# Optimization experiments

Measured on AMD Instinct MI355X. Metric: run time of the kernel, lower is better.

## Reference

```python
import jax, jax.numpy as jnp
import numpy as np


def setup_inputs() -> dict:
    N, E, D = 50000, 800000, 64
    key = jax.random.key(0)
    ks = jax.random.split(key, 8)
    s = 1.0 / np.sqrt(2 * D)
    inp = {
        "node_emb": jax.random.normal(ks[0], (N, D), dtype=jnp.float32),
        "edge_index": jax.random.randint(ks[1], (2, E), 0, N, dtype=jnp.int64),
        "W1": jax.random.normal(ks[2], (2 * D, D), dtype=jnp.float32) * s,
        "b1": jnp.zeros((D,), dtype=jnp.float32),
        "W2": jax.random.normal(ks[3], (D, D), dtype=jnp.float32) * (1.0 / np.sqrt(D)),
        "b2": jnp.zeros((D,), dtype=jnp.float32),
        "Wg": jax.random.normal(ks[4], (D, D), dtype=jnp.float32) * (1.0 / np.sqrt(D)),
        "bg": jnp.zeros((D,), dtype=jnp.float32),
    }
    return inp


def reference(node_emb, edge_index, W1, b1, W2, b2, Wg, bg):
    # Gather pairwise embeddings along edges
    src, dst = edge_index[0], edge_index[1]
    pair_emb = jnp.concatenate([node_emb[src], node_emb[dst]], axis=-1)  # [E, 2D]
    # Interaction MLP (dropout in eval mode -> identity)
    h = jax.nn.relu(pair_emb @ W1 + b1)
    interaction = h @ W2 + b2  # [E, D]
    # Sigmoid gate
    gate = jax.nn.sigmoid(interaction @ Wg + bg)
    gated = interaction * gate  # [E, D]
    # Scatter-mean back to source nodes
    N = node_emb.shape[0]
    summed = jax.ops.segment_sum(gated, src, num_segments=N)  # [N, D]
    counts = jax.ops.segment_sum(jnp.ones((src.shape[0],), dtype=gated.dtype), src, num_segments=N)
    pooled = summed / jnp.maximum(counts, 1.0)[:, None]
    return pooled
```

## Files before the change

### kernel.cpp

```cpp
#include <hip/hip_runtime.h>


typedef unsigned short ushort_t;
typedef __attribute__((ext_vector_type(8))) short     bf16x8;
typedef __attribute__((ext_vector_type(8))) unsigned short u16x8;
typedef __attribute__((ext_vector_type(4))) float     f32x4;

constexpr int D        = 64;
constexpr int TILE     = 64;
constexpr int BLOCK    = 256;
constexpr int NFRAG    = 32;
constexpr int SLAB_B   = 4352;
constexpr int PAIR_STR = 136;
constexpr int H_STR    = 72;
constexpr int G_STR    = 68;

static __device__ __forceinline__ ushort_t f2bf(float f) {
    union { float f; unsigned int u; } v; v.f = f;
    const unsigned int r = v.u + 0x7FFFu + ((v.u >> 16) & 1u);
    return (ushort_t)(r >> 16);
}


__global__ void prep_kernel(const float* __restrict__ W1, const float* __restrict__ W2,
                            const float* __restrict__ Wg,
                            const float* __restrict__ b2, const float* __restrict__ bg,
                            const float* __restrict__ emb, const int* __restrict__ ei,
                            ushort_t* __restrict__ wpack, float* __restrict__ bgp,
                            ushort_t* __restrict__ emb_bf, int* __restrict__ cnt,
                            int total_emb, int cvt_blocks, int E) {
    const int bid = blockIdx.x;
    if (bid < 64) {
        const int t = bid * 256 + threadIdx.x;
        const int f = t >> 9;
        const int l = (t >> 3) & 63;
        const int j = t & 7;
        const int k = ((f < 16) ? (f & 3) : ((f - 16) & 1)) * 32 + (l >> 4) * 8 + j;
        const int n = ((f < 16) ? (f >> 2) : (((f & 7)) >> 1)) * 16 + (l & 15);
        float v;
        if (f < 16)      v = W1[k * 64 + n];
        else if (f < 24) v = W2[k * 64 + n];
        else {
            float s = 0.f;
            const float* wr = W2 + k * 64;
#pragma unroll 8
            for (int m = 0; m < 64; ++m) s += wr[m] * Wg[m * 64 + n];
            v = s;
        }
        wpack[t] = f2bf(v);
    } else if (bid < 64 + cvt_blocks) {
        const int idx  = (bid - 64) * 256 + threadIdx.x;
        const int base = idx * 8;
        if (base < total_emb) {
            const float4 a = *(const float4*)(emb + base);
            const float4 b = *(const float4*)(emb + base + 4);
            u16x8 p;
            p[0]=f2bf(a.x); p[1]=f2bf(a.y); p[2]=f2bf(a.z); p[3]=f2bf(a.w);
            p[4]=f2bf(b.x); p[5]=f2bf(b.y); p[6]=f2bf(b.z); p[7]=f2bf(b.w);
            *(u16x8*)(emb_bf + base) = p;
        }
    } else if (bid == 64 + cvt_blocks) {
        const int n = threadIdx.x;
        if (n < 64) {
            float s = bg[n];
#pragma unroll 8
            for (int m = 0; m < 64; ++m) s += b2[m] * Wg[m * 64 + n];
            bgp[n] = s;
        }
    } else {
        const int e = ((bid - 65 - cvt_blocks) * 256 + threadIdx.x) * 4;
        if (e + 3 < E) {
            const int4 v = *(const int4*)(ei + e);
            atomicAdd(&cnt[v.x], 1); atomicAdd(&cnt[v.y], 1);
            atomicAdd(&cnt[v.z], 1); atomicAdd(&cnt[v.w], 1);
        } else {
            for (int k = e; k < E; ++k) atomicAdd(&cnt[ei[k]], 1);
        }
    }
}


__global__ void scan_block(const int* __restrict__ cnt, int* __restrict__ off,
                           int* __restrict__ bsum, int N) {
    __shared__ int s[256];
    const int t = threadIdx.x, i = blockIdx.x * 256 + t;
    const int x = (i < N) ? cnt[i] : 0;
    s[t] = x; __syncthreads();
    for (int d = 1; d < 256; d <<= 1) {
        const int v = (t >= d) ? s[t - d] : 0;
        __syncthreads();
        s[t] += v;
        __syncthreads();
    }
    if (i < N) off[i] = s[t] - x;
    if (t == 255) bsum[blockIdx.x] = s[255];
}

__global__ void scatter_idx(const int* __restrict__ ei, int* __restrict__ off,
                            const int* __restrict__ bsum, unsigned* __restrict__ sorted,
                            int E, int nb) {
    __shared__ int pref[256];
    const int t = threadIdx.x;
    const int x = (t < nb) ? bsum[t] : 0;
    pref[t] = x; __syncthreads();
    for (int d = 1; d < 256; d <<= 1) {
        const int v = (t >= d) ? pref[t - d] : 0;
        __syncthreads();
        pref[t] += v;
        __syncthreads();
    }
    const int e = (blockIdx.x * blockDim.x + t) * 4;
    if (e + 3 < E) {
        const int4 v = *(const int4*)(ei + e);
        const int4 d = *(const int4*)(ei + E + e);
        const int bx = v.x >> 8, by = v.y >> 8, bz = v.z >> 8, bw = v.w >> 8;
        sorted[(bx ? pref[bx - 1] : 0) + atomicAdd(&off[v.x], 1)] =
            ((unsigned)v.x << 16) | (unsigned)d.x;
        sorted[(by ? pref[by - 1] : 0) + atomicAdd(&off[v.y], 1)] =
            ((unsigned)v.y << 16) | (unsigned)d.y;
        sorted[(bz ? pref[bz - 1] : 0) + atomicAdd(&off[v.z], 1)] =
            ((unsigned)v.z << 16) | (unsigned)d.z;
        sorted[(bw ? pref[bw - 1] : 0) + atomicAdd(&off[v.w], 1)] =
            ((unsigned)v.w << 16) | (unsigned)d.w;
    } else {
        for (int k = e; k < E; ++k) {
            const int s = ei[k], b = s >> 8;
            sorted[(b ? pref[b - 1] : 0) + atomicAdd(&off[s], 1)] =
                ((unsigned)s << 16) | (unsigned)ei[E + k];
        }
    }
}


__global__ __launch_bounds__(BLOCK, 6)
void edge_mlp_mfma(const ushort_t* __restrict__ emb_bf,
                   const unsigned* __restrict__ sorted,
                   const ushort_t* __restrict__ wpack,
                   const float* __restrict__ b1, const float* __restrict__ b2,
                   const float* __restrict__ bgp,
                   const int*   __restrict__ cnt,
                   float* __restrict__ summed,
                   int E)
{
    __shared__ char  slab[4][SLAB_B];
    __shared__ int   srcIds[TILE];
    __shared__ float rcS[TILE];

    const int tid = threadIdx.x;

    {
        const int e = tid >> 2, q = tid & 3;
        ushort_t* prow = (ushort_t*)&slab[e >> 4][(e & 15) * (PAIR_STR * 2)];
        const int ide = blockIdx.x * TILE + e;
        if (ide < E) {
            const unsigned p = sorted[ide];
            const int s  = (int)(p >> 16);
            const int dn = (int)(p & 0xFFFFu);
            if (q == 0) { srcIds[e] = s; rcS[e] = 1.0f / fmaxf((float)cnt[s], 1.0f); }
            const ushort_t* sr = emb_bf + (size_t)s  * D + q * 16;
            const ushort_t* dr = emb_bf + (size_t)dn * D + q * 16;
            *(u16x8*)&prow[q * 16]          = *(const u16x8*)sr;
            *(u16x8*)&prow[q * 16 + 8]      = *(const u16x8*)(sr + 8);
            *(u16x8*)&prow[64 + q * 16]     = *(const u16x8*)dr;
            *(u16x8*)&prow[64 + q * 16 + 8] = *(const u16x8*)(dr + 8);
        } else {
            if (q == 0) { srcIds[e] = -1; rcS[e] = 1.0f; }
            const u16x8 z = {0,0,0,0,0,0,0,0};
            *(u16x8*)&prow[q * 16]          = z;
            *(u16x8*)&prow[q * 16 + 8]      = z;
            *(u16x8*)&prow[64 + q * 16]     = z;
            *(u16x8*)&prow[64 + q * 16 + 8] = z;
        }
    }

    const int w    = tid >> 6;
    const int ln   = tid & 63;
    const int quad = ln >> 4;
    const int cn   = ln & 15;
    ushort_t* pairW = (ushort_t*)slab[w];
    ushort_t* hW    = (ushort_t*)slab[w];
    float*    gW    = (float*)   slab[w];

    bf16x8 a1f[4];
#pragma unroll
    for (int kc = 0; kc < 4; ++kc)
        a1f[kc] = *(const bf16x8*)&pairW[cn * PAIR_STR + kc * 32 + quad * 8];

    f32x4 acc1[4];
#pragma unroll
    for (int nt = 0; nt < 4; ++nt) {
        const float b = b1[nt * 16 + cn];
        acc1[nt] = (f32x4){b, b, b, b};
    }
#pragma unroll
    for (int nt = 0; nt < 4; ++nt)
#pragma unroll
        for (int kc = 0; kc < 4; ++kc) {
            const bf16x8 bf = *(const bf16x8*)(wpack + ((nt * 4 + kc) * 64 + ln) * 8);
            acc1[nt] = __builtin_amdgcn_mfma_f32_16x16x32_bf16(a1f[kc], bf, acc1[nt], 0, 0, 0);
        }
#pragma unroll
    for (int nt = 0; nt < 4; ++nt)
#pragma unroll
        for (int r = 0; r < 4; ++r)
            hW[(quad * 4 + r) * H_STR + nt * 16 + cn] = f2bf(fmaxf(acc1[nt][r], 0.f));

    bf16x8 a2f[2];
#pragma unroll
    for (int kc = 0; kc < 2; ++kc)
        a2f[kc] = *(const bf16x8*)&hW[cn * H_STR + kc * 32 + quad * 8];

    f32x4 acc2[4], accg[4];
#pragma unroll
    for (int nt = 0; nt < 4; ++nt) {
        const float b  = b2 [nt * 16 + cn];
        const float bG = bgp[nt * 16 + cn];
        acc2[nt] = (f32x4){b, b, b, b};
        accg[nt] = (f32x4){bG, bG, bG, bG};
    }
#pragma unroll
    for (int nt = 0; nt < 4; ++nt)
#pragma unroll
        for (int kc = 0; kc < 2; ++kc) {
            const bf16x8 bf2 = *(const bf16x8*)(wpack + ((16 + nt * 2 + kc) * 64 + ln) * 8);
            const bf16x8 bfg = *(const bf16x8*)(wpack + ((24 + nt * 2 + kc) * 64 + ln) * 8);
            acc2[nt] = __builtin_amdgcn_mfma_f32_16x16x32_bf16(a2f[kc], bf2, acc2[nt], 0, 0, 0);
            accg[nt] = __builtin_amdgcn_mfma_f32_16x16x32_bf16(a2f[kc], bfg, accg[nt], 0, 0, 0);
        }

#pragma unroll
    for (int nt = 0; nt < 4; ++nt)
#pragma unroll
        for (int r = 0; r < 4; ++r) {
            const float g = 1.0f / (1.0f + __expf(-accg[nt][r]));
            gW[(quad * 4 + r) * G_STR + nt * 16 + cn] = acc2[nt][r] * g;
        }

    {
        const int rbase = 16 * w;
        float run = 0.f;
        int   prev = srcIds[rbase];
        int   lastIdx = rbase;
#pragma unroll
        for (int i = 0; i < 16; ++i) {
            const int s = srcIds[rbase + i];
            const float v = gW[i * G_STR + ln];
            if (s != prev) {
                if (prev >= 0)
                    unsafeAtomicAdd(&summed[(size_t)prev * D + ln], run * rcS[lastIdx]);
                run = 0.f;
                prev = s;
            }
            run += v;
            lastIdx = rbase + i;
        }
        if (prev >= 0)
            unsafeAtomicAdd(&summed[(size_t)prev * D + ln], run * rcS[lastIdx]);
    }
}

extern "C" void kernel_launch(void* const* d_in, const int* in_sizes, int n_in,
                              void* d_out, int out_size, void* d_ws, size_t ws_size,
                              hipStream_t stream) {
    const float* node_emb   = (const float*)d_in[0];
    const int*   edge_index = (const int*)d_in[1];
    const float* W1 = (const float*)d_in[2];
    const float* b1 = (const float*)d_in[3];
    const float* W2 = (const float*)d_in[4];
    const float* b2 = (const float*)d_in[5];
    const float* Wg = (const float*)d_in[6];
    const float* bg = (const float*)d_in[7];

    const int N = in_sizes[0] / D;
    const int E = in_sizes[1] / 2;
    const int total_emb = N * D;

    int* cnt    = (int*)d_ws;
    int* off    = cnt + N;
    int* bsum   = off + N;
    unsigned* sorted = (unsigned*)(bsum + 256);
    float* bgp  = (float*)(sorted + E);
    ushort_t* wpack  = (ushort_t*)(bgp + 64);
    ushort_t* emb_bf = wpack + NFRAG * 512;

    float* summed = (float*)d_out;

    hipMemsetAsync(cnt, 0, sizeof(int) * (size_t)N, stream);
    hipMemsetAsync(summed, 0, sizeof(float) * (size_t)total_emb, stream);

    const int cvt_blocks = (total_emb / 8 + 255) / 256;
    const int e4blocks   = ((E + 3) / 4 + 255) / 256;
    prep_kernel<<<64 + cvt_blocks + 1 + e4blocks, 256, 0, stream>>>(
        W1, W2, Wg, b2, bg, node_emb, edge_index,
        wpack, bgp, emb_bf, cnt, total_emb, cvt_blocks, E);

    const int nblocks = (N + 255) / 256;
    scan_block <<<nblocks, 256, 0, stream>>>(cnt, off, bsum, N);
    scatter_idx<<<e4blocks, 256, 0, stream>>>(edge_index, off, bsum, sorted, E, nblocks);

    const int ntiles = (E + TILE - 1) / TILE;
    edge_mlp_mfma<<<ntiles, BLOCK, 0, stream>>>(emb_bf, sorted, wpack,
                                                b1, b2, bgp, cnt, summed, E);
}
```

Measured before the change: 256.2 us.

## Reduce segments in registers via shuffles, fold output zeroing into prep kernel

The gated values now stay in registers instead of being staged through LDS: each lane accumulates its rows per source segment and cross-quad sums are done with xor shuffles before the atomic add. The memset of the output is replaced by extra zeroing blocks in the prep kernel, which removes one launch. MFMA loops are reordered to load each A fragment just before use, and the launch-bounds occupancy hint rises from 6 to 8 blocks per CU. Together these aim to cut LDS traffic, registers and launch overhead. The cost is extra shuffle work per segment boundary and possible register spilling under the tighter bound.

```diff
diff --git a/kernel.cpp b/kernel.cpp
--- a/kernel.cpp
+++ b/kernel.cpp
@@ -13,7 +13,6 @@
 constexpr int SLAB_B   = 4352;
 constexpr int PAIR_STR = 136;
 constexpr int H_STR    = 72;
-constexpr int G_STR    = 68;
 
 static __device__ __forceinline__ ushort_t f2bf(float f) {
     union { float f; unsigned int u; } v; v.f = f;
@@ -28,7 +27,8 @@
                             const float* __restrict__ emb, const int* __restrict__ ei,
                             ushort_t* __restrict__ wpack, float* __restrict__ bgp,
                             ushort_t* __restrict__ emb_bf, int* __restrict__ cnt,
-                            int total_emb, int cvt_blocks, int E) {
+                            float* __restrict__ summed,
+                            int total_emb, int cvt_blocks, int e4blocks, int E) {
     const int bid = blockIdx.x;
     if (bid < 64) {
         const int t = bid * 256 + threadIdx.x;
@@ -67,7 +67,7 @@
             for (int m = 0; m < 64; ++m) s += b2[m] * Wg[m * 64 + n];
             bgp[n] = s;
         }
-    } else {
+    } else if (bid < 65 + cvt_blocks + e4blocks) {
         const int e = ((bid - 65 - cvt_blocks) * 256 + threadIdx.x) * 4;
         if (e + 3 < E) {
             const int4 v = *(const int4*)(ei + e);
@@ -76,6 +76,11 @@
         } else {
             for (int k = e; k < E; ++k) atomicAdd(&cnt[ei[k]], 1);
         }
+    } else {
+        const int idx  = (bid - 65 - cvt_blocks - e4blocks) * 256 + threadIdx.x;
+        const int base = idx * 4;
+        if (base < total_emb)
+            *(float4*)(summed + base) = (float4){0.f, 0.f, 0.f, 0.f};
     }
 }
 
@@ -132,7 +137,7 @@
 }
 
 
-__global__ __launch_bounds__(BLOCK, 6)
+__global__ __launch_bounds__(BLOCK, 8)
 void edge_mlp_mfma(const ushort_t* __restrict__ emb_bf,
                    const unsigned* __restrict__ sorted,
                    const ushort_t* __restrict__ wpack,
@@ -149,27 +154,27 @@
     const int tid = threadIdx.x;
 
     {
-        const int e = tid >> 2, q = tid & 3;
+        const int e = tid >> 2, q4 = tid & 3;
         ushort_t* prow = (ushort_t*)&slab[e >> 4][(e & 15) * (PAIR_STR * 2)];
         const int ide = blockIdx.x * TILE + e;
         if (ide < E) {
             const unsigned p = sorted[ide];
             const int s  = (int)(p >> 16);
             const int dn = (int)(p & 0xFFFFu);
-            if (q == 0) { srcIds[e] = s; rcS[e] = 1.0f / fmaxf((float)cnt[s], 1.0f); }
-            const ushort_t* sr = emb_bf + (size_t)s  * D + q * 16;
-            const ushort_t* dr = emb_bf + (size_t)dn * D + q * 16;
-            *(u16x8*)&prow[q * 16]          = *(const u16x8*)sr;
-            *(u16x8*)&prow[q * 16 + 8]      = *(const u16x8*)(sr + 8);
-            *(u16x8*)&prow[64 + q * 16]     = *(const u16x8*)dr;
-            *(u16x8*)&prow[64 + q * 16 + 8] = *(const u16x8*)(dr + 8);
+            if (q4 == 0) { srcIds[e] = s; rcS[e] = 1.0f / fmaxf((float)cnt[s], 1.0f); }
+            const ushort_t* sr = emb_bf + (size_t)s  * D + q4 * 16;
+            const ushort_t* dr = emb_bf + (size_t)dn * D + q4 * 16;
+            *(u16x8*)&prow[q4 * 16]          = *(const u16x8*)sr;
+            *(u16x8*)&prow[q4 * 16 + 8]      = *(const u16x8*)(sr + 8);
+            *(u16x8*)&prow[64 + q4 * 16]     = *(const u16x8*)dr;
+            *(u16x8*)&prow[64 + q4 * 16 + 8] = *(const u16x8*)(dr + 8);
         } else {
-            if (q == 0) { srcIds[e] = -1; rcS[e] = 1.0f; }
+            if (q4 == 0) { srcIds[e] = -1; rcS[e] = 1.0f; }
             const u16x8 z = {0,0,0,0,0,0,0,0};
-            *(u16x8*)&prow[q * 16]          = z;
-            *(u16x8*)&prow[q * 16 + 8]      = z;
-            *(u16x8*)&prow[64 + q * 16]     = z;
-            *(u16x8*)&prow[64 + q * 16 + 8] = z;
+            *(u16x8*)&prow[q4 * 16]          = z;
+            *(u16x8*)&prow[q4 * 16 + 8]      = z;
+            *(u16x8*)&prow[64 + q4 * 16]     = z;
+            *(u16x8*)&prow[64 + q4 * 16 + 8] = z;
         }
     }
 
@@ -179,12 +184,6 @@
     const int cn   = ln & 15;
     ushort_t* pairW = (ushort_t*)slab[w];
     ushort_t* hW    = (ushort_t*)slab[w];
-    float*    gW    = (float*)   slab[w];
-
-    bf16x8 a1f[4];
-#pragma unroll
-    for (int kc = 0; kc < 4; ++kc)
-        a1f[kc] = *(const bf16x8*)&pairW[cn * PAIR_STR + kc * 32 + quad * 8];
 
     f32x4 acc1[4];
 #pragma unroll
@@ -193,22 +192,19 @@
         acc1[nt] = (f32x4){b, b, b, b};
     }
 #pragma unroll
-    for (int nt = 0; nt < 4; ++nt)
-#pragma unroll
-        for (int kc = 0; kc < 4; ++kc) {
+    for (int kc = 0; kc < 4; ++kc) {
+        const bf16x8 a = *(const bf16x8*)&pairW[cn * PAIR_STR + kc * 32 + quad * 8];
+#pragma unroll
+        for (int nt = 0; nt < 4; ++nt) {
             const bf16x8 bf = *(const bf16x8*)(wpack + ((nt * 4 + kc) * 64 + ln) * 8);
-            acc1[nt] = __builtin_amdgcn_mfma_f32_16x16x32_bf16(a1f[kc], bf, acc1[nt], 0, 0, 0);
-        }
+            acc1[nt] = __builtin_amdgcn_mfma_f32_16x16x32_bf16(a, bf, acc1[nt], 0, 0, 0);
+        }
+    }
 #pragma unroll
     for (int nt = 0; nt < 4; ++nt)
 #pragma unroll
         for (int r = 0; r < 4; ++r)
             hW[(quad * 4 + r) * H_STR + nt * 16 + cn] = f2bf(fmaxf(acc1[nt][r], 0.f));
-
-    bf16x8 a2f[2];
-#pragma unroll
-    for (int kc = 0; kc < 2; ++kc)
-        a2f[kc] = *(const bf16x8*)&hW[cn * H_STR + kc * 32 + quad * 8];
 
     f32x4 acc2[4], accg[4];
 #pragma unroll
@@ -219,43 +215,66 @@
         accg[nt] = (f32x4){bG, bG, bG, bG};
     }
 #pragma unroll
-    for (int nt = 0; nt < 4; ++nt)
-#pragma unroll
-        for (int kc = 0; kc < 2; ++kc) {
+    for (int kc = 0; kc < 2; ++kc) {
+        const bf16x8 a = *(const bf16x8*)&hW[cn * H_STR + kc * 32 + quad * 8];
+#pragma unroll
+        for (int nt = 0; nt < 4; ++nt) {
             const bf16x8 bf2 = *(const bf16x8*)(wpack + ((16 + nt * 2 + kc) * 64 + ln) * 8);
             const bf16x8 bfg = *(const bf16x8*)(wpack + ((24 + nt * 2 + kc) * 64 + ln) * 8);
-            acc2[nt] = __builtin_amdgcn_mfma_f32_16x16x32_bf16(a2f[kc], bf2, acc2[nt], 0, 0, 0);
-            accg[nt] = __builtin_amdgcn_mfma_f32_16x16x32_bf16(a2f[kc], bfg, accg[nt], 0, 0, 0);
-        }
-
+            acc2[nt] = __builtin_amdgcn_mfma_f32_16x16x32_bf16(a, bf2, acc2[nt], 0, 0, 0);
+            accg[nt] = __builtin_amdgcn_mfma_f32_16x16x32_bf16(a, bfg, accg[nt], 0, 0, 0);
+        }
+    }
+
+    float g[4][4];
 #pragma unroll
     for (int nt = 0; nt < 4; ++nt)
 #pragma unroll
-        for (int r = 0; r < 4; ++r) {
-            const float g = 1.0f / (1.0f + __expf(-accg[nt][r]));
-            gW[(quad * 4 + r) * G_STR + nt * 16 + cn] = acc2[nt][r] * g;
-        }
+        for (int r = 0; r < 4; ++r)
+            g[nt][r] = acc2[nt][r] / (1.0f + __expf(-accg[nt][r]));
 
     {
         const int rbase = 16 * w;
-        float run = 0.f;
-        int   prev = srcIds[rbase];
-        int   lastIdx = rbase;
+        float part0 = 0.f, part1 = 0.f, part2 = 0.f, part3 = 0.f;
+        int   segSrc = srcIds[rbase];
+        int   segRow = 0;
 #pragma unroll
         for (int i = 0; i < 16; ++i) {
             const int s = srcIds[rbase + i];
-            const float v = gW[i * G_STR + ln];
-            if (s != prev) {
-                if (prev >= 0)
-                    unsafeAtomicAdd(&summed[(size_t)prev * D + ln], run * rcS[lastIdx]);
-                run = 0.f;
-                prev = s;
+            if (s != segSrc) {
+                if (segSrc >= 0) {
+                    float t0 = part0, t1 = part1, t2 = part2, t3 = part3;
+                    t0 += __shfl_xor(t0, 16); t0 += __shfl_xor(t0, 32);
+                    t1 += __shfl_xor(t1, 16); t1 += __shfl_xor(t1, 32);
+                    t2 += __shfl_xor(t2, 16); t2 += __shfl_xor(t2, 32);
+                    t3 += __shfl_xor(t3, 16); t3 += __shfl_xor(t3, 32);
+                    const float tot = (quad < 2) ? (quad == 0 ? t0 : t1)
+                                                 : (quad == 2 ? t2 : t3);
+                    unsafeAtomicAdd(&summed[(size_t)segSrc * D + ln],
+                                    tot * rcS[rbase + segRow]);
+                }
+                part0 = part1 = part2 = part3 = 0.f;
+                segSrc = s;
+                segRow = i;
             }
-            run += v;
-            lastIdx = rbase + i;
-        }
-        if (prev >= 0)
-            unsafeAtomicAdd(&summed[(size_t)prev * D + ln], run * rcS[lastIdx]);
+            if ((i >> 2) == quad) {
+                part0 += g[0][i & 3];
+                part1 += g[1][i & 3];
+                part2 += g[2][i & 3];
+                part3 += g[3][i & 3];
+            }
+        }
+        if (segSrc >= 0) {
+            float t0 = part0, t1 = part1, t2 = part2, t3 = part3;
+            t0 += __shfl_xor(t0, 16); t0 += __shfl_xor(t0, 32);
+            t1 += __shfl_xor(t1, 16); t1 += __shfl_xor(t1, 32);
+            t2 += __shfl_xor(t2, 16); t2 += __shfl_xor(t2, 32);
+            t3 += __shfl_xor(t3, 16); t3 += __shfl_xor(t3, 32);
+            const float tot = (quad < 2) ? (quad == 0 ? t0 : t1)
+                                         : (quad == 2 ? t2 : t3);
+            unsafeAtomicAdd(&summed[(size_t)segSrc * D + ln],
+                            tot * rcS[rbase + segRow]);
+        }
     }
 }
 
@@ -286,13 +305,13 @@
     float* summed = (float*)d_out;
 
     hipMemsetAsync(cnt, 0, sizeof(int) * (size_t)N, stream);
-    hipMemsetAsync(summed, 0, sizeof(float) * (size_t)total_emb, stream);
 
     const int cvt_blocks = (total_emb / 8 + 255) / 256;
     const int e4blocks   = ((E + 3) / 4 + 255) / 256;
-    prep_kernel<<<64 + cvt_blocks + 1 + e4blocks, 256, 0, stream>>>(
+    const int zblocks    = (total_emb / 4 + 255) / 256;
+    prep_kernel<<<64 + cvt_blocks + 1 + e4blocks + zblocks, 256, 0, stream>>>(
         W1, W2, Wg, b2, bg, node_emb, edge_index,
-        wpack, bgp, emb_bf, cnt, total_emb, cvt_blocks, E);
+        wpack, bgp, emb_bf, cnt, summed, total_emb, cvt_blocks, e4blocks, E);
 
     const int nblocks = (N + 255) / 256;
     scan_block <<<nblocks, 256, 0, stream>>>(cnt, off, bsum, N);
```

Measured after the change: 245.3 us. 1.04x faster.
